# Kernel optimization log

Measured on AMD Instinct MI355X. Metric: run time of the kernel, lower is better.

Reference implementation:

```python
import jax, jax.numpy as jnp
import numpy as np

K = 3
STRIDE = 1
PAD = 1
GROUPS = 16
EPS = 1e-5


def _conv2d(x, w, b, stride, pad):
    out = jax.lax.conv_general_dilated(
        x, w, (stride, stride), [(pad, pad), (pad, pad)],
        dimension_numbers=("NCHW", "OIHW", "NCHW"))
    return out + b[None, :, None, None]


def setup_inputs() -> dict:
    key = jax.random.key(0)
    ks = jax.random.split(key, 6)
    B, Cin, H, W = 4, 256, 64, 64
    Cout = 256
    x = jax.random.normal(ks[0], (B, Cin, H, W), dtype=jnp.float32)
    # DCNv2 offset/mask-generating conv: 3*K*K = 27 output channels
    w_off = jax.random.normal(ks[1], (3 * K * K, Cin, K, K), dtype=jnp.float32) * 0.01
    b_off = jnp.zeros((3 * K * K,), dtype=jnp.float32)
    # main deformable conv weight/bias
    weight = jax.random.normal(ks[2], (Cout, Cin, K, K), dtype=jnp.float32) * 0.02
    bias = jnp.zeros((Cout,), dtype=jnp.float32)
    # GroupNorm affine params
    gamma = jnp.ones((Cout,), dtype=jnp.float32)
    beta = jnp.zeros((Cout,), dtype=jnp.float32)
    return {"x": x, "w_off": w_off, "b_off": b_off,
            "weight": weight, "bias": bias, "gamma": gamma, "beta": beta}


def reference(x, w_off, b_off, weight, bias, gamma, beta):
    B, Cin, H, W = x.shape
    Cout = weight.shape[0]
    KK = K * K

    # --- offset/mask branch (DCNv2): 18 offsets + 9 sigmoid masks ---
    om = _conv2d(x, w_off, b_off, STRIDE, PAD)          # [B, 27, Ho, Wo]
    Ho, Wo = om.shape[2], om.shape[3]
    off_y, off_x, m = jnp.split(om, 3, axis=1)          # each [B, 9, Ho, Wo]
    mask = jax.nn.sigmoid(m)

    # --- sampling coordinates: base grid + kernel tap + learned offset ---
    kgy = jnp.repeat(jnp.arange(K, dtype=x.dtype), K)   # [9] row of tap
    kgx = jnp.tile(jnp.arange(K, dtype=x.dtype), K)     # [9] col of tap
    base_y = jnp.arange(Ho, dtype=x.dtype) * STRIDE - PAD
    base_x = jnp.arange(Wo, dtype=x.dtype) * STRIDE - PAD
    py = base_y[None, None, :, None] + kgy[None, :, None, None] + off_y  # [B,9,Ho,Wo]
    px = base_x[None, None, None, :] + kgx[None, :, None, None] + off_x  # [B,9,Ho,Wo]

    # --- bilinear sampling with zero padding outside the image ---
    y0 = jnp.floor(py)
    x0 = jnp.floor(px)
    wy1 = py - y0
    wx1 = px - x0

    def gather(img, yy, xx):
        # img [Cin,H,W], yy/xx [9,Ho,Wo] int -> [Cin,9,Ho,Wo]
        return img[:, yy, xx]

    def corner(yi, xi, wy, wx):
        valid = (yi >= 0) & (yi < H) & (xi >= 0) & (xi < W)
        yc = jnp.clip(yi, 0, H - 1).astype(jnp.int32)
        xc = jnp.clip(xi, 0, W - 1).astype(jnp.int32)
        vals = jax.vmap(gather)(x, yc, xc)               # [B,Cin,9,Ho,Wo]
        w_ = (wy * wx * valid.astype(x.dtype))[:, None]   # [B,1,9,Ho,Wo]
        return vals * w_

    sampled = (corner(y0, x0, (1 - wy1), (1 - wx1))
               + corner(y0, x0 + 1, (1 - wy1), wx1)
               + corner(y0 + 1, x0, wy1, (1 - wx1))
               + corner(y0 + 1, x0 + 1, wy1, wx1))       # [B,Cin,9,Ho,Wo]
    sampled = sampled * mask[:, None]                     # modulation

    # --- conv accumulation over taps and input channels ---
    out = jnp.einsum("bckhw,ock->bohw", sampled,
                     weight.reshape(Cout, Cin, KK)) + bias[None, :, None, None]

    # --- GroupNorm(16, Cout) ---
    og = out.reshape(B, GROUPS, Cout // GROUPS, Ho, Wo)
    mu = og.mean(axis=(2, 3, 4), keepdims=True)
    var = og.var(axis=(2, 3, 4), keepdims=True)
    og = (og - mu) * jax.lax.rsqrt(var + EPS)
    out = og.reshape(B, Cout, Ho, Wo) * gamma[None, :, None, None] + beta[None, :, None, None]
    return out
```

## Files before the change

### kernel.cpp

```cpp
#include <hip/hip_runtime.h>
#include <math.h>

#define CIN   256
#define COUT  256
#define H     64
#define W     64
#define HW    4096
#define KK    9
#define KC    2304
#define NOFF  27
#define B_    4
#define EPS   1e-5f
#define OM3S  (B_ * NOFF * HW)

typedef __attribute__((ext_vector_type(4))) float f32x4;
typedef __attribute__((ext_vector_type(8))) short s16x8;

static __device__ __forceinline__ unsigned short f2bf(float f) {
  unsigned u = __builtin_bit_cast(unsigned, f);
  u += 0x7FFF + ((u >> 16) & 1);
  return (unsigned short)(u >> 16);
}
static __device__ __forceinline__ float bflo(unsigned u) {
  return __builtin_bit_cast(float, u << 16);
}
static __device__ __forceinline__ float bfhi(unsigned u) {
  return __builtin_bit_cast(float, u & 0xffff0000u);
}
static __device__ __forceinline__ unsigned packbf(float lo, float hi) {
  unsigned ul = __builtin_bit_cast(unsigned, lo);
  unsigned uh = __builtin_bit_cast(unsigned, hi);
  ul += 0x7FFF + ((ul >> 16) & 1);
  uh += 0x7FFF + ((uh >> 16) & 1);
  return (ul >> 16) | (uh & 0xffff0000u);
}
static __device__ __forceinline__ void gl2lds16(const void* g, void* l) {
  __builtin_amdgcn_global_load_lds(
      (const __attribute__((address_space(1))) unsigned int*)g,
      (__attribute__((address_space(3))) unsigned int*)l, 16, 0, 0);
}

__global__ __launch_bounds__(256) void prep_kernel(
    const float* __restrict__ x, const float* __restrict__ w,
    const float* __restrict__ w_off, unsigned short* __restrict__ xT,
    unsigned short* __restrict__ wBf, unsigned short* __restrict__ wOBf,
    float* __restrict__ gstat) {
  int bi = blockIdx.x;
  int t = threadIdx.x;
  if (bi < 256) {
    __shared__ unsigned short tile[64][272];
    int b = bi >> 6, y = bi & 63;
    const float* src = x + (size_t)b * CIN * HW + y * W;
    for (int r = 0; r < 64; ++r) {
      int idx = r * 256 + t;
      int c = idx >> 6, ww = idx & 63;
      tile[ww][c] = f2bf(src[(size_t)c * HW + ww]);
    }
    __syncthreads();
    unsigned short* dst = xT + ((size_t)(b * 64 + y) * 64) * 256;
    for (int r = 0; r < 8; ++r) {
      int idx = r * 2048 + t * 8;
      int ww = idx >> 8, c = idx & 255;
      *(uint4*)(dst + idx) = *(const uint4*)&tile[ww][c];
    }
  } else if (bi < 544) {
    int pkt = (bi - 256) * 256 + t;
    int lane = pkt & 63;
    int tn = (pkt >> 6) & 15;
    int k2 = pkt >> 10;
    int co = tn * 16 + (lane & 15);
    int kb = k2 * 32 + (lane >> 4) * 8;
    unsigned short v[8];
#pragma unroll
    for (int j = 0; j < 8; ++j) {
      int kk = kb + j;
      int kt = kk >> 8, c = kk & 255;
      v[j] = f2bf(w[(co * 256 + c) * 9 + kt]);
    }
    *(uint4*)&wBf[(size_t)pkt * 8] = *(const uint4*)v;
  } else if (bi < 580) {
    int pkt = (bi - 544) * 256 + t;
    int lane = pkt & 63;
    int tn = (pkt >> 6) & 1;
    int k2 = pkt >> 7;
    int oc = tn * 16 + (lane & 15);
    int kb = k2 * 32 + (lane >> 4) * 8;
    unsigned short v[8];
#pragma unroll
    for (int j = 0; j < 8; ++j) {
      int kk = kb + j;
      int kt = kk >> 8, c = kk & 255;
      v[j] = (oc < NOFF) ? f2bf(w_off[(oc * 256 + c) * 9 + kt]) : (unsigned short)0;
    }
    *(uint4*)&wOBf[(size_t)pkt * 8] = *(const uint4*)v;
  } else {
    if (t < 128) gstat[t] = 0.f;
  }
}

__global__ __launch_bounds__(256) void offconv_mfma_kernel(
    const unsigned short* __restrict__ xT, const unsigned short* __restrict__ wOBf,
    float* __restrict__ om3) {
  int bi = blockIdx.x;
  int ts = bi >> 8;
  int row = bi & 255;
  int b = row >> 6, i = row & 63;
  int t = threadIdx.x, lane = t & 63, wv = t >> 6;
  int lr = lane & 15, lq = lane >> 4;
  int p = wv * 16 + lr;
  const unsigned short* xb = xT + (size_t)b * (HW * 256);
  f32x4 acc[2] = {};

  for (int kc = 0; kc < 3; ++kc) {
    int kt = ts * 3 + kc;
    int ky = kt / 3, kx = kt % 3;
    int yy = i - 1 + ky, xx = p - 1 + kx;
    bool ok = ((unsigned)yy < 64u) && ((unsigned)xx < 64u);
    const unsigned short* ap = xb + ((ok ? yy * 64 + xx : 0) << 8) + lq * 8;
#pragma unroll
    for (int c8 = 0; c8 < 8; ++c8) {
      uint4 av = uint4{0, 0, 0, 0};
      if (ok) av = *(const uint4*)(ap + c8 * 32);
      int k2 = kt * 8 + c8;
      s16x8 a = __builtin_bit_cast(s16x8, av);
      s16x8 b0 = *(const s16x8*)(wOBf + ((((k2 * 2 + 0) << 6) | lane) << 3));
      s16x8 b1 = *(const s16x8*)(wOBf + ((((k2 * 2 + 1) << 6) | lane) << 3));
      acc[0] = __builtin_amdgcn_mfma_f32_16x16x32_bf16(a, b0, acc[0], 0, 0, 0);
      acc[1] = __builtin_amdgcn_mfma_f32_16x16x32_bf16(a, b1, acc[1], 0, 0, 0);
    }
  }
#pragma unroll
  for (int tn = 0; tn < 2; ++tn) {
    int oc = tn * 16 + lr;
    if (oc < NOFF) {
      float* ob = om3 + (size_t)ts * OM3S + ((b * NOFF + oc) << 12) + i * 64 + wv * 16;
#pragma unroll
      for (int r = 0; r < 4; ++r) ob[lq * 4 + r] = acc[tn][r];
    }
  }
}

__global__ __launch_bounds__(256, 2) void sampler_kernel(
    const unsigned short* __restrict__ xT, const float* __restrict__ om3,
    const float* __restrict__ b_off, unsigned short* __restrict__ Aout) {
  __shared__ float tapw[32][KK][4];
  __shared__ int   tapc[32][KK][4];
  int bi = blockIdx.x;
  int b = bi >> 7, i = (bi >> 1) & 63, j0 = (bi & 1) * 32;
  int t = threadIdx.x;
  const unsigned short* xb = xT + (size_t)b * (HW * 256);

  for (int idx = t; idx < 32 * KK; idx += 256) {
    int p = idx / KK, k = idx % KK;
    int pix = i * 64 + j0 + p;
    size_t o = (size_t)(b * NOFF) * HW + pix;
    float offy = om3[o + k * HW] + om3[OM3S + o + k * HW] +
                 om3[2 * OM3S + o + k * HW] + b_off[k];
    float offx = om3[o + (9 + k) * HW] + om3[OM3S + o + (9 + k) * HW] +
                 om3[2 * OM3S + o + (9 + k) * HW] + b_off[9 + k];
    float mval = om3[o + (18 + k) * HW] + om3[OM3S + o + (18 + k) * HW] +
                 om3[2 * OM3S + o + (18 + k) * HW] + b_off[18 + k];
    float mask = 1.f / (1.f + __expf(-mval));
    float py = (float)(i - 1 + k / 3) + offy;
    float px = (float)(j0 + p - 1 + k % 3) + offx;
    float y0f = floorf(py), x0f = floorf(px);
    float wy1 = py - y0f, wx1 = px - x0f;
    int y0 = (int)y0f, x0 = (int)x0f;
    bool y0ok = (unsigned)y0 < 64u, y1ok = (unsigned)(y0 + 1) < 64u;
    bool x0ok = (unsigned)x0 < 64u, x1ok = (unsigned)(x0 + 1) < 64u;
    tapw[p][k][0] = (1.f - wy1) * (1.f - wx1) * mask * (float)(y0ok && x0ok);
    tapw[p][k][1] = (1.f - wy1) * wx1 * mask * (float)(y0ok && x1ok);
    tapw[p][k][2] = wy1 * (1.f - wx1) * mask * (float)(y1ok && x0ok);
    tapw[p][k][3] = wy1 * wx1 * mask * (float)(y1ok && x1ok);
    int y0c = min(max(y0, 0), 63), y1c = min(max(y0 + 1, 0), 63);
    int x0c = min(max(x0, 0), 63), x1c = min(max(x0 + 1, 0), 63);
    tapc[p][k][0] = (y0c * 64 + x0c) * 256;
    tapc[p][k][1] = (x1c - x0c) * 256;
    tapc[p][k][2] = (y1c - y0c) * 64 * 256;
    tapc[p][k][3] = 0;
  }
  __syncthreads();

  int p = t >> 3, s = t & 7;
  int gpix = b * 4096 + i * 64 + j0 + p;
  unsigned short* arow = Aout + (size_t)gpix * KC;

  for (int kt = 0; kt < KK; ++kt) {
    f32x4 tw = *(const f32x4*)&tapw[p][kt][0];
    float w00 = tw[0], w01 = tw[1], w10 = tw[2], w11 = tw[3];
    int4 tc = *(const int4*)&tapc[p][kt][0];
    const unsigned short* c00 = xb + tc.x + s * 8;
    int dx = tc.y, dy = tc.z;
#pragma unroll
    for (int g = 0; g < 4; ++g) {
      int c = g * 64 + s * 8;
      int cc = g * 64;
      uint4 v00 = *(const uint4*)(c00 + cc);
      uint4 v01 = *(const uint4*)(c00 + dx + cc);
      uint4 v10 = *(const uint4*)(c00 + dy + cc);
      uint4 v11 = *(const uint4*)(c00 + dy + dx + cc);
      const unsigned* a00 = (const unsigned*)&v00;
      const unsigned* a01 = (const unsigned*)&v01;
      const unsigned* a10 = (const unsigned*)&v10;
      const unsigned* a11 = (const unsigned*)&v11;
      uint4 res;
      unsigned* rr = (unsigned*)&res;
#pragma unroll
      for (int q = 0; q < 4; ++q) {
        float lo = w00 * bflo(a00[q]) + w01 * bflo(a01[q]) +
                   w10 * bflo(a10[q]) + w11 * bflo(a11[q]);
        float hi = w00 * bfhi(a00[q]) + w01 * bfhi(a01[q]) +
                   w10 * bfhi(a10[q]) + w11 * bfhi(a11[q]);
        rr[q] = packbf(lo, hi);
      }
      *(uint4*)(arow + kt * 256 + c) = res;
    }
  }
}

__global__ __launch_bounds__(256, 1) void gemm_kernel(
    const unsigned short* __restrict__ A, const unsigned short* __restrict__ wBf,
    const float* __restrict__ bias, unsigned short* __restrict__ cvt,
    float* __restrict__ gstat) {
  __shared__ unsigned short At[2][64 * 64];
  int bi = blockIdx.x;
  int m0 = bi * 64;
  int t = threadIdx.x, lane = t & 63, wv = t >> 6;
  int lr = lane & 15, lq = lane >> 4;
  int rowq = lane >> 3, pos = lane & 7;
  int swz = pos ^ rowq;

  const char* Asrc0 = (const char*)A + (size_t)(m0 + wv * 16 + rowq) * 4608 + swz * 16;
  const char* Asrc1 = Asrc0 + 8 * 4608;
  const unsigned short* bb = wBf + ((size_t)(wv * 4) * 64 + lane) * 8;

  f32x4 acc[4][4] = {};
  s16x8 Bf0[2][4], Bf1[2][4];

  gl2lds16(Asrc0, (char*)At[0] + (wv * 16) * 128);
  gl2lds16(Asrc1, (char*)At[0] + (wv * 16 + 8) * 128);
#pragma unroll
  for (int kh = 0; kh < 2; ++kh)
#pragma unroll
    for (int tn = 0; tn < 4; ++tn)
      Bf0[kh][tn] = *(const s16x8*)(bb + (size_t)kh * 8192 + tn * 512);

#pragma unroll 1
  for (int k = 0; k < 36; k += 2) {
    __syncthreads();
    {
      int koff = (k + 1) * 128;
      gl2lds16(Asrc0 + koff, (char*)At[1] + (wv * 16) * 128);
      gl2lds16(Asrc1 + koff, (char*)At[1] + (wv * 16 + 8) * 128);
      int k2b = (k + 1) * 2;
#pragma unroll
      for (int kh = 0; kh < 2; ++kh)
#pragma unroll
        for (int tn = 0; tn < 4; ++tn)
          Bf1[kh][tn] = *(const s16x8*)(bb + (size_t)(k2b + kh) * 8192 + tn * 512);
    }
    {
      const char* buf = (const char*)At[0];
#pragma unroll
      for (int kh = 0; kh < 2; ++kh) {
        s16x8 af[4];
#pragma unroll
        for (int tm = 0; tm < 4; ++tm) {
          int r = tm * 16 + lr;
          af[tm] = *(const s16x8*)(buf + r * 128 + (((kh * 4 + lq) ^ (r & 7)) * 16));
        }
#pragma unroll
        for (int tm = 0; tm < 4; ++tm)
#pragma unroll
          for (int tn = 0; tn < 4; ++tn)
            acc[tm][tn] = __builtin_amdgcn_mfma_f32_16x16x32_bf16(
                af[tm], Bf0[kh][tn], acc[tm][tn], 0, 0, 0);
      }
    }
    __syncthreads();
    if (k + 2 < 36) {
      int koff = (k + 2) * 128;
      gl2lds16(Asrc0 + koff, (char*)At[0] + (wv * 16) * 128);
      gl2lds16(Asrc1 + koff, (char*)At[0] + (wv * 16 + 8) * 128);
      int k2b = (k + 2) * 2;
#pragma unroll
      for (int kh = 0; kh < 2; ++kh)
#pragma unroll
        for (int tn = 0; tn < 4; ++tn)
          Bf0[kh][tn] = *(const s16x8*)(bb + (size_t)(k2b + kh) * 8192 + tn * 512);
    }
    {
      const char* buf = (const char*)At[1];
#pragma unroll
      for (int kh = 0; kh < 2; ++kh) {
        s16x8 af[4];
#pragma unroll
        for (int tm = 0; tm < 4; ++tm) {
          int r = tm * 16 + lr;
          af[tm] = *(const s16x8*)(buf + r * 128 + (((kh * 4 + lq) ^ (r & 7)) * 16));
        }
#pragma unroll
        for (int tm = 0; tm < 4; ++tm)
#pragma unroll
          for (int tn = 0; tn < 4; ++tn)
            acc[tm][tn] = __builtin_amdgcn_mfma_f32_16x16x32_bf16(
                af[tm], Bf1[kh][tn], acc[tm][tn], 0, 0, 0);
      }
    }
  }

  int b = m0 >> 12;
  int poff = m0 & 4095;
#pragma unroll
  for (int tn = 0; tn < 4; ++tn) {
    int co = wv * 64 + tn * 16 + lr;
    float bco = bias[co];
    unsigned short* cvb = cvt + (size_t)(b * COUT + co) * HW + poff;
    float s = 0.f, q = 0.f;
#pragma unroll
    for (int tm = 0; tm < 4; ++tm) {
      ushort4 st;
#pragma unroll
      for (int r = 0; r < 4; ++r) {
        float v = acc[tm][tn][r] + bco;
        s += v;
        q += v * v;
        ((unsigned short*)&st)[r] = f2bf(v);
      }
      *(ushort4*)(cvb + tm * 16 + lq * 4) = st;
    }
#pragma unroll
    for (int off = 32; off > 0; off >>= 1) {
      s += __shfl_down(s, off, 64);
      q += __shfl_down(q, off, 64);
    }
    if (lane == 0) {
      int g = co >> 4;
      atomicAdd(&gstat[(b * 16 + g) * 2 + 0], s);
      atomicAdd(&gstat[(b * 16 + g) * 2 + 1], q);
    }
  }
}

__global__ __launch_bounds__(256) void gn_apply_kernel(
    const unsigned short* __restrict__ convout, const float* __restrict__ gstat,
    const float* __restrict__ gamma, const float* __restrict__ beta,
    float* __restrict__ out) {
  int vid = blockIdx.x * 256 + threadIdx.x;
  int e = vid * 8;
  int b = e >> 20;
  int c = (e >> 12) & 255;
  int g = c >> 4;
  float S = gstat[(b * 16 + g) * 2 + 0];
  float Q = gstat[(b * 16 + g) * 2 + 1];
  float mu = S * (1.f / 65536.f);
  float var = Q * (1.f / 65536.f) - mu * mu;
  float rs = rsqrtf(var + EPS);
  float a = rs * gamma[c];
  float bb = beta[c] - mu * a;
  uint4 v = *(const uint4*)(convout + e);
  const unsigned* u = (const unsigned*)&v;
  float4 o0, o1;
  o0.x = bflo(u[0]) * a + bb;  o0.y = bfhi(u[0]) * a + bb;
  o0.z = bflo(u[1]) * a + bb;  o0.w = bfhi(u[1]) * a + bb;
  o1.x = bflo(u[2]) * a + bb;  o1.y = bfhi(u[2]) * a + bb;
  o1.z = bflo(u[3]) * a + bb;  o1.w = bfhi(u[3]) * a + bb;
  *(float4*)(out + e) = o0;
  *(float4*)(out + e + 4) = o1;
}

extern "C" void kernel_launch(void* const* d_in, const int* in_sizes, int n_in,
                              void* d_out, int out_size, void* d_ws, size_t ws_size,
                              hipStream_t stream) {
  const float* x      = (const float*)d_in[0];
  const float* w_off  = (const float*)d_in[1];
  const float* b_off  = (const float*)d_in[2];
  const float* weight = (const float*)d_in[3];
  const float* bias   = (const float*)d_in[4];
  const float* gamma  = (const float*)d_in[5];
  const float* beta   = (const float*)d_in[6];
  float* out = (float*)d_out;

  float* om3 = (float*)d_ws;
  unsigned short* xT   = (unsigned short*)(om3 + (size_t)3 * OM3S);
  unsigned short* cvt  = xT;
  unsigned short* wBf  = xT + (size_t)B_ * HW * 256;
  unsigned short* wOBf = wBf + (size_t)COUT * KC;
  unsigned short* Abuf = wOBf + (size_t)32 * KC;
  float* gstat = (float*)(Abuf + (size_t)B_ * HW * KC);

  prep_kernel<<<dim3(581), dim3(256), 0, stream>>>(x, weight, w_off, xT, wBf, wOBf, gstat);
  offconv_mfma_kernel<<<dim3(768), dim3(256), 0, stream>>>(xT, wOBf, om3);
  sampler_kernel<<<dim3(512), dim3(256), 0, stream>>>(xT, om3, b_off, Abuf);
  gemm_kernel<<<dim3(256), dim3(256), 0, stream>>>(Abuf, wBf, bias, cvt, gstat);
  gn_apply_kernel<<<dim3(2048), dim3(256), 0, stream>>>(cvt, gstat, gamma, beta, out);
}
```

Measured before the change: 187.6 us.

## Fuse deformable bilinear sampler into the GEMM, sampling A tiles directly into LDS

Merges the sampler and GEMM kernels. Each block now computes a 32-pixel M tile, bilinearly samples the modulated im2col rows straight into double-buffered swizzled LDS, and pipelines the next tap's gathers and B loads with the MFMA work on the current buffer. This removes the write and re-read of the large bf16 im2col buffer in global memory and one kernel launch. The cost is a smaller M tile per block (32 rows instead of 64), so more B-fragment reloads per output, gather latency sitting inside the GEMM loop, and setprio hints around the MFMAs. cvt no longer aliases xT and is placed in a separate workspace region.

```diff
diff --git a/kernel.cpp b/kernel.cpp
--- a/kernel.cpp
+++ b/kernel.cpp
@@ -33,11 +33,6 @@
   ul += 0x7FFF + ((ul >> 16) & 1);
   uh += 0x7FFF + ((uh >> 16) & 1);
   return (ul >> 16) | (uh & 0xffff0000u);
-}
-static __device__ __forceinline__ void gl2lds16(const void* g, void* l) {
-  __builtin_amdgcn_global_load_lds(
-      (const __attribute__((address_space(1))) unsigned int*)g,
-      (__attribute__((address_space(3))) unsigned int*)l, 16, 0, 0);
 }
 
 __global__ __launch_bounds__(256) void prep_kernel(
@@ -140,19 +135,25 @@
   }
 }
 
-__global__ __launch_bounds__(256, 2) void sampler_kernel(
+__global__ __launch_bounds__(256, 2) void gemm_fused_kernel(
     const unsigned short* __restrict__ xT, const float* __restrict__ om3,
-    const float* __restrict__ b_off, unsigned short* __restrict__ Aout) {
+    const float* __restrict__ b_off, const unsigned short* __restrict__ wBf,
+    const float* __restrict__ bias, unsigned short* __restrict__ cvt,
+    float* __restrict__ gstat) {
   __shared__ float tapw[32][KK][4];
   __shared__ int   tapc[32][KK][4];
+  __shared__ unsigned short At[2][32 * 64];
   int bi = blockIdx.x;
-  int b = bi >> 7, i = (bi >> 1) & 63, j0 = (bi & 1) * 32;
-  int t = threadIdx.x;
+  int m0 = bi * 32;
+  int b = m0 >> 12;
+  int i = (m0 & 4095) >> 6, j0 = m0 & 63;
+  int t = threadIdx.x, lane = t & 63, wv = t >> 6;
+  int lr = lane & 15, lq = lane >> 4;
   const unsigned short* xb = xT + (size_t)b * (HW * 256);
 
   for (int idx = t; idx < 32 * KK; idx += 256) {
     int p = idx / KK, k = idx % KK;
-    int pix = i * 64 + j0 + p;
+    int pix = (m0 & 4095) + p;
     size_t o = (size_t)(b * NOFF) * HW + pix;
     float offy = om3[o + k * HW] + om3[OM3S + o + k * HW] +
                  om3[2 * OM3S + o + k * HW] + b_off[k];
@@ -182,164 +183,120 @@
   __syncthreads();
 
   int p = t >> 3, s = t & 7;
-  int gpix = b * 4096 + i * 64 + j0 + p;
-  unsigned short* arow = Aout + (size_t)gpix * KC;
-
-  for (int kt = 0; kt < KK; ++kt) {
-    f32x4 tw = *(const f32x4*)&tapw[p][kt][0];
-    float w00 = tw[0], w01 = tw[1], w10 = tw[2], w11 = tw[3];
-    int4 tc = *(const int4*)&tapc[p][kt][0];
-    const unsigned short* c00 = xb + tc.x + s * 8;
-    int dx = tc.y, dy = tc.z;
-#pragma unroll
-    for (int g = 0; g < 4; ++g) {
-      int c = g * 64 + s * 8;
-      int cc = g * 64;
-      uint4 v00 = *(const uint4*)(c00 + cc);
-      uint4 v01 = *(const uint4*)(c00 + dx + cc);
-      uint4 v10 = *(const uint4*)(c00 + dy + cc);
-      uint4 v11 = *(const uint4*)(c00 + dy + dx + cc);
-      const unsigned* a00 = (const unsigned*)&v00;
-      const unsigned* a01 = (const unsigned*)&v01;
-      const unsigned* a10 = (const unsigned*)&v10;
-      const unsigned* a11 = (const unsigned*)&v11;
-      uint4 res;
-      unsigned* rr = (unsigned*)&res;
-#pragma unroll
-      for (int q = 0; q < 4; ++q) {
-        float lo = w00 * bflo(a00[q]) + w01 * bflo(a01[q]) +
-                   w10 * bflo(a10[q]) + w11 * bflo(a11[q]);
-        float hi = w00 * bfhi(a00[q]) + w01 * bfhi(a01[q]) +
-                   w10 * bfhi(a10[q]) + w11 * bfhi(a11[q]);
-        rr[q] = packbf(lo, hi);
-      }
-      *(uint4*)(arow + kt * 256 + c) = res;
-    }
-  }
-}
-
-__global__ __launch_bounds__(256, 1) void gemm_kernel(
-    const unsigned short* __restrict__ A, const unsigned short* __restrict__ wBf,
-    const float* __restrict__ bias, unsigned short* __restrict__ cvt,
-    float* __restrict__ gstat) {
-  __shared__ unsigned short At[2][64 * 64];
-  int bi = blockIdx.x;
-  int m0 = bi * 64;
-  int t = threadIdx.x, lane = t & 63, wv = t >> 6;
-  int lr = lane & 15, lq = lane >> 4;
-  int rowq = lane >> 3, pos = lane & 7;
-  int swz = pos ^ rowq;
-
-  const char* Asrc0 = (const char*)A + (size_t)(m0 + wv * 16 + rowq) * 4608 + swz * 16;
-  const char* Asrc1 = Asrc0 + 8 * 4608;
   const unsigned short* bb = wBf + ((size_t)(wv * 4) * 64 + lane) * 8;
 
-  f32x4 acc[4][4] = {};
+  f32x4 acc[2][4] = {};
   s16x8 Bf0[2][4], Bf1[2][4];
-
-  gl2lds16(Asrc0, (char*)At[0] + (wv * 16) * 128);
-  gl2lds16(Asrc1, (char*)At[0] + (wv * 16 + 8) * 128);
-#pragma unroll
-  for (int kh = 0; kh < 2; ++kh)
-#pragma unroll
-    for (int tn = 0; tn < 4; ++tn)
-      Bf0[kh][tn] = *(const s16x8*)(bb + (size_t)kh * 8192 + tn * 512);
+  uint4 g00, g01, g10, g11;
+  f32x4 tw;
+
+#define PLOAD(KSUB)                                                          \
+  {                                                                          \
+    int kt_ = (KSUB) >> 2, cg_ = (KSUB) & 3;                                 \
+    tw = *(const f32x4*)&tapw[p][kt_][0];                                    \
+    int4 tc_ = *(const int4*)&tapc[p][kt_][0];                               \
+    const unsigned short* c00_ = xb + tc_.x + cg_ * 64 + s * 8;              \
+    g00 = *(const uint4*)(c00_);                                             \
+    g01 = *(const uint4*)(c00_ + tc_.y);                                     \
+    g10 = *(const uint4*)(c00_ + tc_.z);                                     \
+    g11 = *(const uint4*)(c00_ + tc_.z + tc_.y);                             \
+  }
+
+#define PSTORE(BUFI)                                                         \
+  {                                                                          \
+    const unsigned* a00_ = (const unsigned*)&g00;                            \
+    const unsigned* a01_ = (const unsigned*)&g01;                            \
+    const unsigned* a10_ = (const unsigned*)&g10;                            \
+    const unsigned* a11_ = (const unsigned*)&g11;                            \
+    uint4 res_;                                                              \
+    unsigned* rr_ = (unsigned*)&res_;                                        \
+    _Pragma("unroll") for (int q = 0; q < 4; ++q) {                          \
+      float lo_ = tw[0] * bflo(a00_[q]) + tw[1] * bflo(a01_[q]) +            \
+                  tw[2] * bflo(a10_[q]) + tw[3] * bflo(a11_[q]);             \
+      float hi_ = tw[0] * bfhi(a00_[q]) + tw[1] * bfhi(a01_[q]) +            \
+                  tw[2] * bfhi(a10_[q]) + tw[3] * bfhi(a11_[q]);             \
+      rr_[q] = packbf(lo_, hi_);                                             \
+    }                                                                        \
+    *(uint4*)((char*)At[BUFI] + p * 128 + ((s ^ (p & 7)) * 16)) = res_;      \
+  }
+
+#define LOADB(BF, K2B)                                                       \
+  _Pragma("unroll") for (int kh = 0; kh < 2; ++kh)                           \
+  _Pragma("unroll") for (int tn = 0; tn < 4; ++tn)                           \
+      BF[kh][tn] = *(const s16x8*)(bb + (size_t)((K2B) + kh) * 8192 + tn * 512);
+
+#define CONSUME(BUFI, BF)                                                    \
+  {                                                                          \
+    const char* buf_ = (const char*)At[BUFI];                                \
+    _Pragma("unroll") for (int kh = 0; kh < 2; ++kh) {                       \
+      s16x8 af0 = *(const s16x8*)(buf_ + lr * 128 + (((kh * 4 + lq) ^ (lr & 7)) * 16)); \
+      s16x8 af1 = *(const s16x8*)(buf_ + (16 + lr) * 128 + (((kh * 4 + lq) ^ (lr & 7)) * 16)); \
+      __builtin_amdgcn_s_setprio(1);                                         \
+      _Pragma("unroll") for (int tn = 0; tn < 4; ++tn) {                     \
+        acc[0][tn] = __builtin_amdgcn_mfma_f32_16x16x32_bf16(                \
+            af0, BF[kh][tn], acc[0][tn], 0, 0, 0);                           \
+        acc[1][tn] = __builtin_amdgcn_mfma_f32_16x16x32_bf16(                \
+            af1, BF[kh][tn], acc[1][tn], 0, 0, 0);                           \
+      }                                                                      \
+      __builtin_amdgcn_s_setprio(0);                                         \
+    }                                                                        \
+  }
+
+  PLOAD(0);
+  PSTORE(0);
+  LOADB(Bf0, 0);
+  __syncthreads();
 
 #pragma unroll 1
   for (int k = 0; k < 36; k += 2) {
-    __syncthreads();
-    {
-      int koff = (k + 1) * 128;
-      gl2lds16(Asrc0 + koff, (char*)At[1] + (wv * 16) * 128);
-      gl2lds16(Asrc1 + koff, (char*)At[1] + (wv * 16 + 8) * 128);
-      int k2b = (k + 1) * 2;
-#pragma unroll
-      for (int kh = 0; kh < 2; ++kh)
-#pragma unroll
-        for (int tn = 0; tn < 4; ++tn)
-          Bf1[kh][tn] = *(const s16x8*)(bb + (size_t)(k2b + kh) * 8192 + tn * 512);
-    }
-    {
-      const char* buf = (const char*)At[0];
-#pragma unroll
-      for (int kh = 0; kh < 2; ++kh) {
-        s16x8 af[4];
-#pragma unroll
-        for (int tm = 0; tm < 4; ++tm) {
-          int r = tm * 16 + lr;
-          af[tm] = *(const s16x8*)(buf + r * 128 + (((kh * 4 + lq) ^ (r & 7)) * 16));
-        }
-#pragma unroll
-        for (int tm = 0; tm < 4; ++tm)
-#pragma unroll
-          for (int tn = 0; tn < 4; ++tn)
-            acc[tm][tn] = __builtin_amdgcn_mfma_f32_16x16x32_bf16(
-                af[tm], Bf0[kh][tn], acc[tm][tn], 0, 0, 0);
-      }
-    }
+    PLOAD(k + 1);
+    LOADB(Bf1, (k + 1) * 2);
+    CONSUME(0, Bf0);
+    PSTORE(1);
     __syncthreads();
     if (k + 2 < 36) {
-      int koff = (k + 2) * 128;
-      gl2lds16(Asrc0 + koff, (char*)At[0] + (wv * 16) * 128);
-      gl2lds16(Asrc1 + koff, (char*)At[0] + (wv * 16 + 8) * 128);
-      int k2b = (k + 2) * 2;
-#pragma unroll
-      for (int kh = 0; kh < 2; ++kh)
-#pragma unroll
-        for (int tn = 0; tn < 4; ++tn)
-          Bf0[kh][tn] = *(const s16x8*)(bb + (size_t)(k2b + kh) * 8192 + tn * 512);
-    }
-    {
-      const char* buf = (const char*)At[1];
-#pragma unroll
-      for (int kh = 0; kh < 2; ++kh) {
-        s16x8 af[4];
-#pragma unroll
-        for (int tm = 0; tm < 4; ++tm) {
-          int r = tm * 16 + lr;
-          af[tm] = *(const s16x8*)(buf + r * 128 + (((kh * 4 + lq) ^ (r & 7)) * 16));
-        }
-#pragma unroll
-        for (int tm = 0; tm < 4; ++tm)
-#pragma unroll
-          for (int tn = 0; tn < 4; ++tn)
-            acc[tm][tn] = __builtin_amdgcn_mfma_f32_16x16x32_bf16(
-                af[tm], Bf1[kh][tn], acc[tm][tn], 0, 0, 0);
-      }
-    }
-  }
-
-  int b = m0 >> 12;
+      PLOAD(k + 2);
+      LOADB(Bf0, (k + 2) * 2);
+    }
+    CONSUME(1, Bf1);
+    if (k + 2 < 36) PSTORE(0);
+    __syncthreads();
+  }
+
   int poff = m0 & 4095;
 #pragma unroll
   for (int tn = 0; tn < 4; ++tn) {
     int co = wv * 64 + tn * 16 + lr;
     float bco = bias[co];
     unsigned short* cvb = cvt + (size_t)(b * COUT + co) * HW + poff;
-    float s = 0.f, q = 0.f;
-#pragma unroll
-    for (int tm = 0; tm < 4; ++tm) {
+    float sS = 0.f, qQ = 0.f;
+#pragma unroll
+    for (int tm = 0; tm < 2; ++tm) {
       ushort4 st;
 #pragma unroll
       for (int r = 0; r < 4; ++r) {
         float v = acc[tm][tn][r] + bco;
-        s += v;
-        q += v * v;
+        sS += v;
+        qQ += v * v;
         ((unsigned short*)&st)[r] = f2bf(v);
       }
       *(ushort4*)(cvb + tm * 16 + lq * 4) = st;
     }
 #pragma unroll
     for (int off = 32; off > 0; off >>= 1) {
-      s += __shfl_down(s, off, 64);
-      q += __shfl_down(q, off, 64);
+      sS += __shfl_down(sS, off, 64);
+      qQ += __shfl_down(qQ, off, 64);
     }
     if (lane == 0) {
       int g = co >> 4;
-      atomicAdd(&gstat[(b * 16 + g) * 2 + 0], s);
-      atomicAdd(&gstat[(b * 16 + g) * 2 + 1], q);
-    }
-  }
+      atomicAdd(&gstat[(b * 16 + g) * 2 + 0], sS);
+      atomicAdd(&gstat[(b * 16 + g) * 2 + 1], qQ);
+    }
+  }
+#undef PLOAD
+#undef PSTORE
+#undef LOADB
+#undef CONSUME
 }
 
 __global__ __launch_bounds__(256) void gn_apply_kernel(
@@ -383,15 +340,13 @@
 
   float* om3 = (float*)d_ws;
   unsigned short* xT   = (unsigned short*)(om3 + (size_t)3 * OM3S);
-  unsigned short* cvt  = xT;
   unsigned short* wBf  = xT + (size_t)B_ * HW * 256;
   unsigned short* wOBf = wBf + (size_t)COUT * KC;
-  unsigned short* Abuf = wOBf + (size_t)32 * KC;
-  float* gstat = (float*)(Abuf + (size_t)B_ * HW * KC);
+  unsigned short* cvt  = wOBf + (size_t)32 * KC;
+  float* gstat = (float*)(cvt + (size_t)B_ * HW * KC);
 
   prep_kernel<<<dim3(581), dim3(256), 0, stream>>>(x, weight, w_off, xT, wBf, wOBf, gstat);
   offconv_mfma_kernel<<<dim3(768), dim3(256), 0, stream>>>(xT, wOBf, om3);
-  sampler_kernel<<<dim3(512), dim3(256), 0, stream>>>(xT, om3, b_off, Abuf);
-  gemm_kernel<<<dim3(256), dim3(256), 0, stream>>>(Abuf, wBf, bias, cvt, gstat);
+  gemm_fused_kernel<<<dim3(512), dim3(256), 0, stream>>>(xT, om3, b_off, wBf, bias, cvt, gstat);
   gn_apply_kernel<<<dim3(2048), dim3(256), 0, stream>>>(cvt, gstat, gamma, beta, out);
 }
```

After: 216.2 us. 1.15x slower.
